# Kernel tuning notes

Hardware: AMD Instinct MI355X
Metric: run time of the kernel (lower is better)

The kernel has to match this reference:

```python
import jax, jax.numpy as jnp
import numpy as np

CONF_THRES = 0.25
IOU_THRES = 0.45
MAX_DET = 300      # max detections returned (padded/masked to static shape)
K = 8192           # top-K score candidates entering NMS (static bound)
N_ANCHORS = 102000 # YOLOv5 @ 1280px
NC = 80            # COCO classes


def setup_inputs() -> dict:
    key = jax.random.key(0)
    # [B=1, N, 4 (xywh) + 1 (obj) + 80 (cls)] raw head predictions in [0,1)
    preds = jax.random.uniform(key, (1, N_ANCHORS, 4 + 1 + NC), dtype=jnp.float32)
    return {"preds": preds}


def _xywh2yxyx(b):
    # (xc, yc, w, h) -> (y1, x1, y2, x2), matching pt_xywh2yxyx_yolo
    x, y, w, h = b[..., 0], b[..., 1], b[..., 2], b[..., 3]
    return jnp.stack([y - h * 0.5, x - w * 0.5, y + h * 0.5, x + w * 0.5], axis=-1)


def _iou_matrix(boxes):
    # boxes: [K, 4] in yxyx; returns pairwise IoU [K, K]
    area = (boxes[:, 2] - boxes[:, 0]) * (boxes[:, 3] - boxes[:, 1])
    ty = jnp.maximum(boxes[:, None, 0], boxes[None, :, 0])
    tx = jnp.maximum(boxes[:, None, 1], boxes[None, :, 1])
    by = jnp.minimum(boxes[:, None, 2], boxes[None, :, 2])
    bx = jnp.minimum(boxes[:, None, 3], boxes[None, :, 3])
    inter = jnp.clip(by - ty, 0.0) * jnp.clip(bx - tx, 0.0)
    union = area[:, None] + area[None, :] - inter
    return inter / (union + 1e-9)


def _yolo_nms(preds):
    p = preds[0]                       # [N, 85] (loop returns on first image)
    obj = p[:, 4]                      # objectness
    cand = obj > CONF_THRES            # confidence filter
    cls_scores = p[:, 5:] * obj[:, None]
    scores = jnp.max(cls_scores, axis=1)
    classes = jnp.argmax(cls_scores, axis=1).astype(jnp.float32)
    scores = jnp.where(cand, scores, 0.0)  # mask instead of dynamic filter
    boxes = _xywh2yxyx(p[:, :4])       # [N, 4] yxyx

    # top-K candidates by score (static replacement for boolean filtering)
    top_scores, idx = jax.lax.top_k(scores, K)
    top_boxes = boxes[idx]
    top_classes = classes[idx]
    valid = top_scores > 0.0

    iou = _iou_matrix(top_boxes)       # [K, K], 256 MB fp32

    # greedy NMS: boxes already sorted by descending score
    ar = jnp.arange(K)

    def body(i, suppressed):
        keep_i = jnp.logical_and(jnp.logical_not(suppressed[i]), valid[i])
        return suppressed | (keep_i & (iou[i] > IOU_THRES) & (ar > i))

    suppressed = jax.lax.fori_loop(0, K, body, jnp.zeros((K,), jnp.bool_))
    keep = valid & jnp.logical_not(suppressed)

    # gather top MAX_DET kept detections (sorted), zero-pad the rest
    keep_scores = jnp.where(keep, top_scores, -1.0)
    _, sel = jax.lax.top_k(keep_scores, MAX_DET)
    mask = keep[sel]
    out_boxes = jnp.where(mask[:, None], top_boxes[sel], 0.0)[None]    # [1, MAX_DET, 4]
    out_classes = jnp.where(mask, top_classes[sel], 0.0)[None]         # [1, MAX_DET]
    out_scores = jnp.where(mask, top_scores[sel], 0.0)[None]           # [1, MAX_DET]
    return out_boxes, out_classes, out_scores


def reference(preds):
    return _yolo_nms(preds)
```

## Files before the change

### kernel.cpp

```cpp
#include <hip/hip_runtime.h>
#include <cstdint>

#define CONF_THRES 0.25f
#define IOU_THRES  0.45f
#define MAX_DET    300
#define K_TOP      8192
#define NA         102000
#define NCLS       80
#define ROWLEN     85
#define CAP        32640
#define NPLANE     32
#define NBINS      16384
#define WIN        512
#define NWIN       (K_TOP / WIN)
#define SSTR       9

typedef unsigned long long u64;
typedef unsigned int u32;

__global__ __launch_bounds__(256) void zero_kernel(uint4* __restrict__ a,
        uint4* __restrict__ r, uint4* __restrict__ b) {
    int i = blockIdx.x * 256 + threadIdx.x;
    uint4 z = make_uint4(0u, 0u, 0u, 0u);
    if (i < 4164) a[i] = z;
    if (i < 8160) r[i] = z;
    b[i] = z;
    b[i + 65536] = z;
}

__global__ __launch_bounds__(256) void score_key_kernel(const float* __restrict__ preds,
        u64* __restrict__ keys, u32* __restrict__ histP) {
#pragma clang fp contract(off)
    int lane = threadIdx.x & 63;
    int i = blockIdx.x * 4 + (threadIdx.x >> 6);
    if (i >= NA) return;
    const float* p = preds + (size_t)i * ROWLEN;
    float v0 = p[lane];
    float v1 = (lane < ROWLEN - 64) ? p[64 + lane] : 0.0f;
    float obj = __shfl(v0, 4);
    float m = (lane >= 5) ? v0 : 0.0f;
    m = fmaxf(m, (lane < 21) ? v1 : 0.0f);
    for (int off = 32; off; off >>= 1) m = fmaxf(m, __shfl_xor(m, off));
    if (lane == 0) {
        float score = (obj > CONF_THRES) ? m * obj : 0.0f;
        u32 sb = __float_as_uint(score);
        keys[i] = ((u64)sb << 32) | (u32)(~(u32)i);
        if (sb != 0u)
            atomicAdd(&histP[((u32)blockIdx.x & (NPLANE - 1u)) * NBINS + (sb >> 16)], 1u);
    }
}

__global__ __launch_bounds__(256) void reduce_hist_kernel(const u32* __restrict__ histP,
        u32* __restrict__ sumhist) {
    int bin = blockIdx.x * 256 + threadIdx.x;
    u32 s = 0;
#pragma unroll
    for (int r = 0; r < NPLANE; ++r) s += histP[r * NBINS + bin];
    sumhist[bin] = s;
}

__global__ __launch_bounds__(1024) void cutoff_kernel(const u32* __restrict__ hist,
        u32* __restrict__ meta) {
    __shared__ u32 suf[1024];
    __shared__ int cbs;
    __shared__ u32 above_s;
    int t = threadIdx.x;
    u32 s = 0;
    const u32* hb = hist + t * 16;
    for (int b = 0; b < 16; ++b) s += hb[b];
    suf[t] = s;
    if (t == 0) { cbs = -1; above_s = 0; }
    __syncthreads();
    for (int off = 1; off < 1024; off <<= 1) {
        u32 add = (t + off < 1024) ? suf[t + off] : 0u;
        __syncthreads();
        suf[t] += add;
        __syncthreads();
    }
    u32 st = suf[t];
    u32 stn = (t < 1023) ? suf[t + 1] : 0u;
    if (st >= (u32)K_TOP && stn < (u32)K_TOP) {
        cbs = t;
        above_s = stn;
    }
    __syncthreads();
    int cb = cbs;
    if (t < 64) {
        u32 thresh = 0;
        if (cb >= 0) {
            u32 above = above_s;
            u32 v = (t < 16) ? hist[cb * 16 + t] : 0u;
            for (int off = 1; off < 64; off <<= 1) {
                u32 o = __shfl_down(v, off);
                if (t + off < 64) v += o;
            }
            u64 bal = __ballot(v + above >= (u32)K_TOP);
            int bstar = 63 - __builtin_clzll((unsigned long long)bal);
            thresh = ((u32)(cb * 16 + bstar)) << 16;
        }
        if (t == 0) meta[1] = thresh;
    }
}

__global__ __launch_bounds__(256) void compact_kernel(const u64* __restrict__ keys,
        u32* __restrict__ meta, u64* __restrict__ comp) {
    __shared__ u32 woff[4];
    __shared__ u32 bbase;
    int i = blockIdx.x * 256 + threadIdx.x;
    int wid = threadIdx.x >> 6, lane = threadIdx.x & 63;
    u64 key = (i < NA) ? keys[i] : 0ull;
    u32 sb = (u32)(key >> 32);
    u32 th = meta[1];
    bool take = (i < NA) && (sb != 0u) && (sb >= th);
    u64 bal = __ballot(take);
    if (lane == 0) woff[wid] = (u32)__popcll(bal);
    __syncthreads();
    if (threadIdx.x == 0) {
        u32 t0 = woff[0], t1 = woff[1], t2 = woff[2], t3 = woff[3];
        bbase = atomicAdd(&meta[0], t0 + t1 + t2 + t3);
        woff[0] = 0; woff[1] = t0; woff[2] = t0 + t1; woff[3] = t0 + t1 + t2;
    }
    __syncthreads();
    if (take) {
        u32 pos = bbase + woff[wid] + (u32)__popcll(bal & ((1ull << lane) - 1ull));
        if (pos < CAP) comp[pos] = key;
    }
}

__global__ __launch_bounds__(256) void rank_partial_kernel(const u64* __restrict__ comp,
        const u32* __restrict__ meta, u32* __restrict__ rankArr) {
    __shared__ u64 tile[1024];
    u32 cnt = meta[0];
    int n = (int)(cnt < (u32)CAP ? cnt : (u32)CAP);
    int i0 = blockIdx.x * 256;
    int j0 = blockIdx.y * 1024;
    if (i0 >= n || j0 >= n) return;
    int lim = n - j0; if (lim > 1024) lim = 1024;
    for (int k = threadIdx.x; k < 1024; k += 256)
        tile[k] = (k < lim) ? comp[j0 + k] : 0ull;
    __syncthreads();
    int i = i0 + threadIdx.x;
    if (i < n) {
        u64 key = comp[i];
        u32 r = 0;
#pragma unroll 8
        for (int j = 0; j < 1024; ++j) r += (tile[j] > key) ? 1u : 0u;
        atomicAdd(&rankArr[i], r);
    }
}

__global__ __launch_bounds__(256) void scatter_kernel(const u64* __restrict__ comp,
        const u32* __restrict__ meta, const u32* __restrict__ rankArr,
        u64* __restrict__ sorted) {
    u32 cnt = meta[0];
    int n = (int)(cnt < (u32)CAP ? cnt : (u32)CAP);
    int i = blockIdx.x * 256 + threadIdx.x;
    if (i < n) {
        u32 r = rankArr[i];
        if (r < (u32)K_TOP) sorted[r] = comp[i];
    }
}

__global__ __launch_bounds__(256) void gather_kernel(const u64* __restrict__ sorted,
        const float* __restrict__ preds, float* __restrict__ boxes,
        float* __restrict__ scores, float* __restrict__ classes,
        float* __restrict__ areas) {
#pragma clang fp contract(off)
    int lane = threadIdx.x & 63;
    int i = blockIdx.x * 4 + (threadIdx.x >> 6);
    u64 key = sorted[i];
    u32 sb = (u32)(key >> 32);
    float score = __uint_as_float(sb);
    if (score > 0.0f) {
        u32 idx = ~(u32)(key & 0xffffffffull);
        const float* p = preds + (size_t)idx * ROWLEN;
        float v0 = p[lane];
        float v1 = (lane < ROWLEN - 64) ? p[64 + lane] : 0.0f;
        float obj = __shfl(v0, 4);
        u64 kb = 0;
        if (lane >= 5) {
            float q = v0 * obj;
            kb = ((u64)__float_as_uint(q) << 8) | (u32)(255 - (lane - 5));
        }
        if (lane < 21) {
            float q = v1 * obj;
            u64 kb2 = ((u64)__float_as_uint(q) << 8) | (u32)(255 - (59 + lane));
            if (kb2 > kb) kb = kb2;
        }
        for (int off = 32; off; off >>= 1) {
            u64 o = __shfl_xor(kb, off);
            if (o > kb) kb = o;
        }
        u32 cls = 255u - (u32)(kb & 0xffull);
        float x = __shfl(v0, 0), y = __shfl(v0, 1);
        float w = __shfl(v0, 2), h = __shfl(v0, 3);
        if (lane == 0) {
            float ymin = y - h * 0.5f, xmin = x - w * 0.5f;
            float ymax = y + h * 0.5f, xmax = x + w * 0.5f;
            boxes[i * 4 + 0] = ymin;
            boxes[i * 4 + 1] = xmin;
            boxes[i * 4 + 2] = ymax;
            boxes[i * 4 + 3] = xmax;
            scores[i] = score;
            classes[i] = (float)cls;
            areas[i] = (ymax - ymin) * (xmax - xmin);
        }
    } else if (lane == 0) {
        boxes[i * 4 + 0] = 0.0f; boxes[i * 4 + 1] = 0.0f;
        boxes[i * 4 + 2] = 0.0f; boxes[i * 4 + 3] = 0.0f;
        scores[i] = 0.0f;
        classes[i] = 0.0f;
        areas[i] = 0.0f;
    }
}

__global__ __launch_bounds__(256) void mask_kernel(const float* __restrict__ boxes,
        const float* __restrict__ areas, const float* __restrict__ scores,
        u64* __restrict__ mask, u64* __restrict__ remw) {
#pragma clang fp contract(off)
    int cx = blockIdx.x;
    int ry = blockIdx.y;
    if (cx < (ry >> 2)) return;
    __shared__ float4 cb[256];
    __shared__ float  ca[256];
    __shared__ u64 st[64 * 5];
    int tid = threadIdx.x;
    int wv = tid >> 6, lane = tid & 63;
    int r0 = ry * 64;
    int jw = cx * 4 + wv;
    cb[tid] = ((const float4*)boxes)[cx * 256 + tid];
    ca[tid] = areas[cx * 256 + tid];
    if (cx == (ry >> 2) && wv == 0) {
        u64 b = __ballot(scores[r0 + lane] > 0.0f);
        if (lane == 0) remw[ry] = b;
    }
    __syncthreads();
    u64 myword = 0;
    if (jw >= ry) {
        float4 bi = ((const float4*)boxes)[r0 + lane];
        float ai = areas[r0 + lane];
        const double Bd = (double)IOU_THRES + 0x1p-26;
        int kb = wv * 64;
#pragma unroll
        for (int k = 0; k < 64; ++k) {
            float4 bj = cb[kb + k];
            float aj = ca[kb + k];
            float ty = fmaxf(bi.x, bj.x);
            float tx = fmaxf(bi.y, bj.y);
            float by = fminf(bi.z, bj.z);
            float bx = fminf(bi.w, bj.w);
            float inter = fmaxf(by - ty, 0.0f) * fmaxf(bx - tx, 0.0f);
            float uni = (ai + aj) - inter;
            float u = uni + 1e-9f;
            bool sup = ((double)inter > Bd * (double)u);
            myword |= sup ? (1ull << k) : 0ull;
        }
        if (jw == ry)
            myword &= (lane < 63) ? (~0ull << (lane + 1)) : 0ull;
    }
    st[lane * 5 + wv] = myword;
    __syncthreads();
    mask[(size_t)(r0 + (tid >> 2)) * 128 + cx * 4 + (tid & 3)] =
            st[(tid >> 2) * 5 + (tid & 3)];
}

__device__ __forceinline__ u64 rfl64(u64 v) {
    u32 lo = (u32)__builtin_amdgcn_readfirstlane((int)(u32)v);
    u32 hi = (u32)__builtin_amdgcn_readfirstlane((int)(u32)(v >> 32));
    return ((u64)hi << 32) | lo;
}

__device__ __forceinline__ u64 bcast64(u64 v, int srclane) {
    u32 lo = (u32)__builtin_amdgcn_readlane((int)(u32)v, srclane);
    u32 hi = (u32)__builtin_amdgcn_readlane((int)(u32)(v >> 32), srclane);
    return ((u64)hi << 32) | lo;
}

__device__ __forceinline__ u64 shfl_xor64(u64 v, int m) {
    u32 lo = __shfl_xor((u32)v, m, 64);
    u32 hi = __shfl_xor((u32)(v >> 32), m, 64);
    return ((u64)hi << 32) | lo;
}

__global__ __launch_bounds__(64) void nms_scan_kernel(const u64* __restrict__ mask,
        const u64* __restrict__ remw, const float* __restrict__ boxes,
        const float* __restrict__ scores, const float* __restrict__ classes,
        float* __restrict__ out) {
    __shared__ u64 sub[WIN * SSTR];
    __shared__ u32 ki[MAX_DET + 8];
    int lane = threadIdx.x;
    int n = 0;
    for (int win = 0; win < NWIN && n < MAX_DET; ++win) {
        int rbase = win * WIN;
        __syncthreads();
#pragma unroll 8
        for (int it = 0; it < 32; ++it) {
            int idx = it * 64 + lane;
            int r = idx >> 2, j = (idx & 3) * 2;
            uint4 v = *(const uint4*)&mask[(size_t)(rbase + r) * 128 + win * 8 + j];
            sub[r * SSTR + j]     = ((u64)v.y << 32) | v.x;
            sub[r * SSTR + j + 1] = ((u64)v.w << 32) | v.z;
        }
        u64 acc[8] = {0, 0, 0, 0, 0, 0, 0, 0};
        for (int m = lane; m < n; m += 64) {
            int k = (int)ki[m];
            const u64* rp = &mask[(size_t)k * 128 + win * 8];
#pragma unroll
            for (int j = 0; j < 8; ++j) acc[j] |= rp[j];
        }
#pragma unroll
        for (int j = 0; j < 8; ++j)
            for (int off = 32; off; off >>= 1) acc[j] |= shfl_xor64(acc[j], off);
        __syncthreads();
        u64 diag[8];
#pragma unroll
        for (int sw = 0; sw < 8; ++sw) diag[sw] = sub[(sw * 64 + lane) * SSTR + sw];
        int n0 = n;
        u64 keptW[8] = {0, 0, 0, 0, 0, 0, 0, 0};
#pragma unroll
        for (int sw = 0; sw < 8; ++sw) {
            if (n < MAX_DET) {
                u64 acc2 = 0;
#pragma unroll
                for (int wp = 0; wp < 8; ++wp) {
                    if (wp < sw) {
                        if ((keptW[wp] >> lane) & 1ull)
                            acc2 |= sub[(wp * 64 + lane) * SSTR + sw];
                    }
                }
                for (int off = 32; off; off >>= 1) acc2 |= shfl_xor64(acc2, off);
                u64 cur = rfl64(remw[win * 8 + sw]) & ~rfl64(acc[sw]) & ~rfl64(acc2);
                u64 kw = 0;
                while (cur != 0ull && n < MAX_DET) {
                    int b = __ffsll((unsigned long long)cur) - 1;
                    u64 slice = bcast64(diag[sw], b);
                    kw |= (1ull << b);
                    cur &= ~(slice | (1ull << b));
                    ++n;
                }
                keptW[sw] = kw;
            }
        }
        int base = n0;
#pragma unroll
        for (int sw = 0; sw < 8; ++sw) {
            u64 kw = keptW[sw];
            if ((kw >> lane) & 1ull) {
                int rr = (int)__popcll(kw & ((1ull << lane) - 1ull));
                ki[base + rr] = (u32)(rbase + sw * 64 + lane);
            }
            base += (int)__popcll(kw);
        }
        __syncthreads();
    }
    __syncthreads();
    for (int m = lane; m < MAX_DET; m += 64) {
        float4 b = make_float4(0.0f, 0.0f, 0.0f, 0.0f);
        float c = 0.0f, s = 0.0f;
        if (m < n) {
            int k = (int)ki[m];
            b = ((const float4*)boxes)[k];
            c = classes[k];
            s = scores[k];
        }
        ((float4*)out)[m] = b;
        out[1200 + m] = c;
        out[1500 + m] = s;
    }
}

extern "C" void kernel_launch(void* const* d_in, const int* in_sizes, int n_in,
                              void* d_out, int out_size, void* d_ws, size_t ws_size,
                              hipStream_t stream) {
    const float* preds = (const float*)d_in[0];
    char* ws = (char*)d_ws;

    u32*   sumhist = (u32*)(ws + 0);
    u32*   rankArr = (u32*)(ws + 65536);
    u32*   meta    = (u32*)(ws + 262144);
    u64*   remw    = (u64*)(ws + 262208);
    u64*   sorted  = (u64*)(ws + 263232);
    u64*   keys    = (u64*)(ws + 328768);
    u64*   comp    = (u64*)(ws + 1144768);
    float* careas  = (float*)(ws + 1144768);
    float* tboxes  = (float*)(ws + 1405888);
    float* tscores = (float*)(ws + 1536960);
    float* tclass  = (float*)(ws + 1569728);
    u64*   mask    = (u64*)(ws + 1602496);
    u32*   histP   = (u32*)(ws + 1602496);
    float* out     = (float*)d_out;

    zero_kernel<<<256, 256, 0, stream>>>((uint4*)(ws + 262144), (uint4*)rankArr,
            (uint4*)histP);
    score_key_kernel<<<(NA + 3) / 4, 256, 0, stream>>>(preds, keys, histP);
    reduce_hist_kernel<<<64, 256, 0, stream>>>(histP, sumhist);
    cutoff_kernel<<<1, 1024, 0, stream>>>(sumhist, meta);
    compact_kernel<<<(NA + 255) / 256, 256, 0, stream>>>(keys, meta, comp);
    rank_partial_kernel<<<dim3((CAP + 255) / 256, (CAP + 1023) / 1024), 256, 0, stream>>>(
            comp, meta, rankArr);
    scatter_kernel<<<(CAP + 255) / 256, 256, 0, stream>>>(comp, meta, rankArr, sorted);
    gather_kernel<<<K_TOP / 4, 256, 0, stream>>>(sorted, preds, tboxes, tscores,
            tclass, careas);
    mask_kernel<<<dim3(32, 128), 256, 0, stream>>>(tboxes, careas, tscores, mask, remw);
    nms_scan_kernel<<<1, 64, 0, stream>>>(mask, remw, tboxes, tscores, tclass, out);
}
```

Measured before the change: 196.4 us.

## Double-buffer NMS scan windows with producer waves and shrink histogram planes

The serial NMS scan kernel grows from one wave to four. Three waves prefetch the next 512-row mask window into a second shared buffer while wave 0 runs the greedy scan on the current one, and all four waves share the OR-reduction over previously kept rows. NPLANE also drops from 32 to 8, which halves the zeroing kernel's work and presumably reduces histogram-plane reduction cost. The trade-offs are more histogram atomic contention in the score kernel, an extra barrier per window, and a larger shared-memory footprint.

```diff
diff --git a/kernel.cpp b/kernel.cpp
--- a/kernel.cpp
+++ b/kernel.cpp
@@ -9,7 +9,7 @@
 #define NCLS       80
 #define ROWLEN     85
 #define CAP        32640
-#define NPLANE     32
+#define NPLANE     8
 #define NBINS      16384
 #define WIN        512
 #define NWIN       (K_TOP / WIN)
@@ -25,7 +25,6 @@
     if (i < 4164) a[i] = z;
     if (i < 8160) r[i] = z;
     b[i] = z;
-    b[i + 65536] = z;
 }
 
 __global__ __launch_bounds__(256) void score_key_kernel(const float* __restrict__ preds,
@@ -282,27 +281,33 @@
     return ((u64)hi << 32) | lo;
 }
 
-__global__ __launch_bounds__(64) void nms_scan_kernel(const u64* __restrict__ mask,
+__global__ __launch_bounds__(256) void nms_scan_kernel(const u64* __restrict__ mask,
         const u64* __restrict__ remw, const float* __restrict__ boxes,
         const float* __restrict__ scores, const float* __restrict__ classes,
         float* __restrict__ out) {
-    __shared__ u64 sub[WIN * SSTR];
+    __shared__ u64 sub[2][WIN * SSTR];
+    __shared__ u64 accW[4][8];
     __shared__ u32 ki[MAX_DET + 8];
-    int lane = threadIdx.x;
+    __shared__ int n_sh;
+    int tid = threadIdx.x;
+    int wid = tid >> 6, lane = tid & 63;
+    if (tid == 0) n_sh = 0;
+#pragma unroll
+    for (int it = 0; it < 8; ++it) {
+        int idx = it * 256 + tid;
+        int r = idx >> 2, j = (idx & 3) * 2;
+        uint4 v = *(const uint4*)&mask[(size_t)r * 128 + j];
+        sub[0][r * SSTR + j]     = ((u64)v.y << 32) | v.x;
+        sub[0][r * SSTR + j + 1] = ((u64)v.w << 32) | v.z;
+    }
+    __syncthreads();
     int n = 0;
-    for (int win = 0; win < NWIN && n < MAX_DET; ++win) {
+    for (int win = 0; win < NWIN; ++win) {
+        if (n >= MAX_DET) break;
         int rbase = win * WIN;
-        __syncthreads();
-#pragma unroll 8
-        for (int it = 0; it < 32; ++it) {
-            int idx = it * 64 + lane;
-            int r = idx >> 2, j = (idx & 3) * 2;
-            uint4 v = *(const uint4*)&mask[(size_t)(rbase + r) * 128 + win * 8 + j];
-            sub[r * SSTR + j]     = ((u64)v.y << 32) | v.x;
-            sub[r * SSTR + j + 1] = ((u64)v.w << 32) | v.z;
-        }
+        int cb = win & 1;
         u64 acc[8] = {0, 0, 0, 0, 0, 0, 0, 0};
-        for (int m = lane; m < n; m += 64) {
+        for (int m = tid; m < n; m += 256) {
             int k = (int)ki[m];
             const u64* rp = &mask[(size_t)k * 128 + win * 8];
 #pragma unroll
@@ -311,50 +316,74 @@
 #pragma unroll
         for (int j = 0; j < 8; ++j)
             for (int off = 32; off; off >>= 1) acc[j] |= shfl_xor64(acc[j], off);
+        if (lane == 0) {
+#pragma unroll
+            for (int j = 0; j < 8; ++j) accW[wid][j] = acc[j];
+        }
         __syncthreads();
-        u64 diag[8];
-#pragma unroll
-        for (int sw = 0; sw < 8; ++sw) diag[sw] = sub[(sw * 64 + lane) * SSTR + sw];
-        int n0 = n;
-        u64 keptW[8] = {0, 0, 0, 0, 0, 0, 0, 0};
-#pragma unroll
-        for (int sw = 0; sw < 8; ++sw) {
-            if (n < MAX_DET) {
-                u64 acc2 = 0;
-#pragma unroll
-                for (int wp = 0; wp < 8; ++wp) {
-                    if (wp < sw) {
-                        if ((keptW[wp] >> lane) & 1ull)
-                            acc2 |= sub[(wp * 64 + lane) * SSTR + sw];
+        if (wid != 0) {
+            if (win + 1 < NWIN) {
+                int t = tid - 64;
+                for (int it = 0; it < 11; ++it) {
+                    int idx = it * 192 + t;
+                    if (idx < 2048) {
+                        int r = idx >> 2, j = (idx & 3) * 2;
+                        uint4 v = *(const uint4*)&mask[
+                                (size_t)(rbase + WIN + r) * 128 + (win + 1) * 8 + j];
+                        sub[cb ^ 1][r * SSTR + j]     = ((u64)v.y << 32) | v.x;
+                        sub[cb ^ 1][r * SSTR + j + 1] = ((u64)v.w << 32) | v.z;
                     }
                 }
-                for (int off = 32; off; off >>= 1) acc2 |= shfl_xor64(acc2, off);
-                u64 cur = rfl64(remw[win * 8 + sw]) & ~rfl64(acc[sw]) & ~rfl64(acc2);
-                u64 kw = 0;
-                while (cur != 0ull && n < MAX_DET) {
-                    int b = __ffsll((unsigned long long)cur) - 1;
-                    u64 slice = bcast64(diag[sw], b);
-                    kw |= (1ull << b);
-                    cur &= ~(slice | (1ull << b));
-                    ++n;
+            }
+        } else {
+            u64 diag[8];
+#pragma unroll
+            for (int sw = 0; sw < 8; ++sw)
+                diag[sw] = sub[cb][(sw * 64 + lane) * SSTR + sw];
+            int n0 = n;
+            u64 keptW[8] = {0, 0, 0, 0, 0, 0, 0, 0};
+#pragma unroll
+            for (int sw = 0; sw < 8; ++sw) {
+                if (n < MAX_DET) {
+                    u64 acc2 = 0;
+#pragma unroll
+                    for (int wp = 0; wp < 8; ++wp) {
+                        if (wp < sw) {
+                            if ((keptW[wp] >> lane) & 1ull)
+                                acc2 |= sub[cb][(wp * 64 + lane) * SSTR + sw];
+                        }
+                    }
+                    for (int off = 32; off; off >>= 1) acc2 |= shfl_xor64(acc2, off);
+                    u64 afold = accW[0][sw] | accW[1][sw] | accW[2][sw] | accW[3][sw];
+                    u64 cur = rfl64(remw[win * 8 + sw]) & ~rfl64(afold) & ~rfl64(acc2);
+                    u64 kw = 0;
+                    while (cur != 0ull && n < MAX_DET) {
+                        int b = __ffsll((unsigned long long)cur) - 1;
+                        u64 slice = bcast64(diag[sw], b);
+                        kw |= (1ull << b);
+                        cur &= ~(slice | (1ull << b));
+                        ++n;
+                    }
+                    keptW[sw] = kw;
                 }
-                keptW[sw] = kw;
             }
-        }
-        int base = n0;
-#pragma unroll
-        for (int sw = 0; sw < 8; ++sw) {
-            u64 kw = keptW[sw];
-            if ((kw >> lane) & 1ull) {
-                int rr = (int)__popcll(kw & ((1ull << lane) - 1ull));
-                ki[base + rr] = (u32)(rbase + sw * 64 + lane);
+            int base = n0;
+#pragma unroll
+            for (int sw = 0; sw < 8; ++sw) {
+                u64 kw = keptW[sw];
+                if ((kw >> lane) & 1ull) {
+                    int rr = (int)__popcll(kw & ((1ull << lane) - 1ull));
+                    ki[base + rr] = (u32)(rbase + sw * 64 + lane);
+                }
+                base += (int)__popcll(kw);
             }
-            base += (int)__popcll(kw);
+            if (lane == 0) n_sh = n;
         }
         __syncthreads();
-    }
-    __syncthreads();
-    for (int m = lane; m < MAX_DET; m += 64) {
+        n = n_sh;
+    }
+    __syncthreads();
+    for (int m = tid; m < MAX_DET; m += 256) {
         float4 b = make_float4(0.0f, 0.0f, 0.0f, 0.0f);
         float c = 0.0f, s = 0.0f;
         if (m < n) {
@@ -390,7 +419,7 @@
     u32*   histP   = (u32*)(ws + 1602496);
     float* out     = (float*)d_out;
 
-    zero_kernel<<<256, 256, 0, stream>>>((uint4*)(ws + 262144), (uint4*)rankArr,
+    zero_kernel<<<128, 256, 0, stream>>>((uint4*)(ws + 262144), (uint4*)rankArr,
             (uint4*)histP);
     score_key_kernel<<<(NA + 3) / 4, 256, 0, stream>>>(preds, keys, histP);
     reduce_hist_kernel<<<64, 256, 0, stream>>>(histP, sumhist);
@@ -402,5 +431,5 @@
     gather_kernel<<<K_TOP / 4, 256, 0, stream>>>(sorted, preds, tboxes, tscores,
             tclass, careas);
     mask_kernel<<<dim3(32, 128), 256, 0, stream>>>(tboxes, careas, tscores, mask, remw);
-    nms_scan_kernel<<<1, 64, 0, stream>>>(mask, remw, tboxes, tscores, tclass, out);
-}
+    nms_scan_kernel<<<1, 256, 0, stream>>>(mask, remw, tboxes, tscores, tclass, out);
+}
```

Measured after the change: 193.3 us. No clear change (-1.6%).
